# Performance work log

Hardware: AMD Instinct MI355X
Metric: run time of the kernel (lower is better)

The kernel has to match this reference:

```python
import jax, jax.numpy as jnp
import numpy as np

N = 50000          # num nodes
E = 600000         # num edges
D_IN = 128         # node_dim
D_HID = 128        # hidden_dim
D_OUT = 32         # num_classes
R = 32             # num_relations
B = 8              # num_bases


def setup_inputs() -> dict:
    key = jax.random.key(0)
    ks = jax.random.split(key, 12)
    inp = {
        "x": jax.random.normal(ks[0], (N, D_IN), dtype=jnp.float32),
        "V1": jax.random.normal(ks[1], (B, D_IN, D_HID), dtype=jnp.float32) * 0.05,
        "a1": jax.random.normal(ks[2], (R, B), dtype=jnp.float32),
        "root1": jax.random.normal(ks[3], (D_IN, D_HID), dtype=jnp.float32) * 0.05,
        "bias1": jnp.zeros((D_HID,), dtype=jnp.float32),
        "V2": jax.random.normal(ks[4], (B, D_HID, D_OUT), dtype=jnp.float32) * 0.05,
        "a2": jax.random.normal(ks[5], (R, B), dtype=jnp.float32),
        "root2": jax.random.normal(ks[6], (D_HID, D_OUT), dtype=jnp.float32) * 0.05,
        "bias2": jnp.zeros((D_OUT,), dtype=jnp.float32),
        "edge_index": jax.random.randint(ks[7], (2, E), 0, N, dtype=jnp.int64),
        "edge_type": jax.random.randint(ks[8], (E,), 0, R, dtype=jnp.int64),
    }
    return inp


def rgcn_layer(x, V, a, root, bias, src, dst, etype):
    # Aggregate neighbor features per (relation, dst-node) with mean norm,
    # then apply basis-decomposed relation weights W_r = sum_b a[r,b] V_b.
    D = x.shape[-1]
    seg = etype * N + dst                                   # [E] combined segment id
    msgs = x[src]                                           # [E, D] gather
    agg = jax.ops.segment_sum(msgs, seg, num_segments=R * N)        # [R*N, D]
    cnt = jax.ops.segment_sum(jnp.ones((msgs.shape[0], 1), x.dtype), seg,
                              num_segments=R * N)                   # [R*N, 1]
    agg = (agg / jnp.maximum(cnt, 1.0)).reshape(R, N, D)            # [R, N, D]
    W = jnp.einsum('rb,bdo->rdo', a, V)                     # [R, D, Dout]
    out = jnp.einsum('rnd,rdo->no', agg, W) + x @ root + bias
    return out


def reference(x, V1, a1, root1, bias1, V2, a2, root2, bias2, edge_index, edge_type):
    src, dst = edge_index[0], edge_index[1]
    h = rgcn_layer(x, V1, a1, root1, bias1, src, dst, edge_type)
    h = jax.nn.relu(h)
    h = rgcn_layer(h, V2, a2, root2, bias2, src, dst, edge_type)
    return jax.nn.softmax(h, axis=1)
```

## Files before the change

kernel.cpp:

```cpp
#include <hip/hip_runtime.h>
#include <hip/hip_bf16.h>


typedef __attribute__((ext_vector_type(8))) short bf16x8;
typedef __attribute__((ext_vector_type(4))) float f32x4;
typedef unsigned short u16;

constexpr int TD   = 128;
constexpr int TB   = 8;
constexpr int TK   = TB * TD;
constexpr int TNB  = 16;
constexpr int BLK  = 512;
constexpr int ZK   = TK + 8;
constexpr int XK   = TD + 8;

__device__ inline void splitbf(float v, u16& h, u16& l) {
  unsigned int u = __float_as_uint(v);
  unsigned int r = u + 0x7FFF + ((u >> 16) & 1);
  u16 hb = (u16)(r >> 16);
  float hv = __uint_as_float((unsigned int)hb << 16);
  float lo = v - hv;
  unsigned int u2 = __float_as_uint(lo);
  unsigned int r2 = u2 + 0x7FFF + ((u2 >> 16) & 1);
  h = hb;
  l = (u16)(r2 >> 16);
}

__global__ void k_prep(const float* __restrict__ V1, const float* __restrict__ root1,
                       const float* __restrict__ V2, const float* __restrict__ root2,
                       u16* __restrict__ v1th, u16* __restrict__ v1tl,
                       u16* __restrict__ r1th, u16* __restrict__ r1tl,
                       u16* __restrict__ v2th, u16* __restrict__ v2tl,
                       u16* __restrict__ r2th, u16* __restrict__ r2tl) {
  int idx = blockIdx.x * 256 + threadIdx.x;
  if (idx < 128 * 1024) splitbf(V1[(size_t)(idx & 1023) * 128 + (idx >> 10)], v1th[idx], v1tl[idx]);
  if (idx < 128 * 128)  splitbf(root1[(size_t)(idx & 127) * 128 + (idx >> 7)], r1th[idx], r1tl[idx]);
  if (idx < 32 * 1024)  splitbf(V2[(size_t)(idx & 1023) * 32 + (idx >> 10)], v2th[idx], v2tl[idx]);
  if (idx < 32 * 128)   splitbf(root2[(size_t)(idx & 127) * 32 + (idx >> 7)], r2th[idx], r2tl[idx]);
}

__global__ void k_hist(const int* __restrict__ ei, const int* __restrict__ et,
                       int* __restrict__ deg, int* __restrict__ cnt2,
                       int E, int N) {
  int e = blockIdx.x * 256 + threadIdx.x;
  if (e >= E) return;
  int d = ei[E + e];
  int r = et[e];
  atomicAdd(&deg[d], 1);
  atomicAdd(&cnt2[r * N + d], 1);
}

__global__ void k_scan(const int* __restrict__ deg, int* __restrict__ off,
                       int* __restrict__ cursor, int n, int total) {
  __shared__ int wsum[16];
  __shared__ int carry_s;
  const int t = threadIdx.x, lane = t & 63, w = t >> 6;
  if (t == 0) carry_s = 0;
  __syncthreads();
  for (int base = 0; base < n; base += 1024) {
    int i = base + t;
    int v = (i < n) ? deg[i] : 0;
    int s = v;
#pragma unroll
    for (int d = 1; d < 64; d <<= 1) {
      int u = __shfl_up(s, d);
      if (lane >= d) s += u;
    }
    if (lane == 63) wsum[w] = s;
    __syncthreads();
    if (w == 0) {
      int ws = (lane < 16) ? wsum[lane] : 0;
#pragma unroll
      for (int d = 1; d < 16; d <<= 1) {
        int u = __shfl_up(ws, d);
        if (lane >= d) ws += u;
      }
      if (lane < 16) wsum[lane] = ws;
    }
    __syncthreads();
    int wbase = (w == 0) ? 0 : wsum[w - 1];
    int carry = carry_s;
    if (i < n) { int ex = carry + wbase + s - v; off[i] = ex; cursor[i] = ex; }
    __syncthreads();
    if (t == 1023) carry_s = carry + wbase + s;
    __syncthreads();
  }
  if (t == 0) off[n] = total;
}

__global__ void k_scatter(const int* __restrict__ ei, const int* __restrict__ et,
                          int* __restrict__ cursor, const int* __restrict__ cnt2,
                          int* __restrict__ packed, float* __restrict__ invc,
                          int E, int N) {
  int e = blockIdx.x * 256 + threadIdx.x;
  if (e >= E) return;
  int s = ei[e], d = ei[E + e], r = et[e];
  int p = atomicAdd(&cursor[d], 1);
  packed[p] = s | (r << 17);
  invc[p] = 1.0f / (float)cnt2[r * N + d];
}

#define MFMA16(A, B, C) __builtin_amdgcn_mfma_f32_16x16x32_bf16((A), (B), (C), 0, 0, 0)

template <int DOUT, bool RELU, bool SOFTMAX>
__global__ __launch_bounds__(BLK, 4) void k_layer(
    const float* __restrict__ in,
    const u16* __restrict__ wth, const u16* __restrict__ wtl,
    const float* __restrict__ a,
    const u16* __restrict__ rth, const u16* __restrict__ rtl,
    const float* __restrict__ bias, const int* __restrict__ off,
    const int* __restrict__ packed, const float* __restrict__ invc,
    float* __restrict__ out, int Ntot) {
  extern __shared__ char smem[];
  u16* zh = (u16*)smem;
  u16* zl = zh + TNB * ZK;
  u16* xh = zl + TNB * ZK;
  u16* xl2 = xh + TNB * XK;
  float* ash = (float*)(xl2 + TNB * XK);
  const int t = threadIdx.x;
  const int n0 = blockIdx.x * TNB;

  if (t < 256) ash[t] = a[t];
  {
    int row = t >> 5;
    int c4 = (t & 31) * 4;
    int n = n0 + row;
    float4 v = make_float4(0.f, 0.f, 0.f, 0.f);
    if (n < Ntot) v = *reinterpret_cast<const float4*>(in + (size_t)n * TD + c4);
    u16 h0, l0;
    splitbf(v.x, h0, l0); xh[row * XK + c4]     = h0; xl2[row * XK + c4]     = l0;
    splitbf(v.y, h0, l0); xh[row * XK + c4 + 1] = h0; xl2[row * XK + c4 + 1] = l0;
    splitbf(v.z, h0, l0); xh[row * XK + c4 + 2] = h0; xl2[row * XK + c4 + 2] = l0;
    splitbf(v.w, h0, l0); xh[row * XK + c4 + 3] = h0; xl2[row * XK + c4 + 3] = l0;
  }
  __syncthreads();

  {
    const int wv = t >> 6, lane = t & 63;
    for (int nn = wv * 2; nn < wv * 2 + 2; ++nn) {
      int n = n0 + nn;
      float zacc[16];
#pragma unroll
      for (int j = 0; j < 16; ++j) zacc[j] = 0.f;
      if (n < Ntot) {
        int e = off[n], e1 = off[n + 1];
        for (; e + 2 <= e1; e += 2) {
          int pk0 = packed[e], pk1 = packed[e + 1];
          float iv0 = invc[e], iv1 = invc[e + 1];
          int s0 = pk0 & 131071, r0 = pk0 >> 17;
          int s1 = pk1 & 131071, r1 = pk1 >> 17;
          float x00 = in[(size_t)s0 * TD + lane];
          float x01 = in[(size_t)s0 * TD + 64 + lane];
          float x10 = in[(size_t)s1 * TD + lane];
          float x11 = in[(size_t)s1 * TD + 64 + lane];
          const float* ar0 = ash + r0 * TB;
          const float* ar1 = ash + r1 * TB;
#pragma unroll
          for (int b = 0; b < TB; ++b) {
            float c0 = ar0[b] * iv0;
            float c1 = ar1[b] * iv1;
            zacc[2 * b]     += c0 * x00;
            zacc[2 * b + 1] += c0 * x01;
            zacc[2 * b]     += c1 * x10;
            zacc[2 * b + 1] += c1 * x11;
          }
        }
        if (e < e1) {
          int pk = packed[e];
          float iv = invc[e];
          int s = pk & 131071, r = pk >> 17;
          float xv0 = in[(size_t)s * TD + lane];
          float xv1 = in[(size_t)s * TD + 64 + lane];
          const float* ar = ash + r * TB;
#pragma unroll
          for (int b = 0; b < TB; ++b) {
            float c = ar[b] * iv;
            zacc[2 * b]     += c * xv0;
            zacc[2 * b + 1] += c * xv1;
          }
        }
      }
#pragma unroll
      for (int b = 0; b < TB; ++b) {
        u16 h0, l0, h1, l1;
        splitbf(zacc[2 * b], h0, l0);
        splitbf(zacc[2 * b + 1], h1, l1);
        zh[nn * ZK + b * TD + lane]      = h0;
        zl[nn * ZK + b * TD + lane]      = l0;
        zh[nn * ZK + b * TD + 64 + lane] = h1;
        zl[nn * ZK + b * TD + 64 + lane] = l1;
      }
    }
  }
  __syncthreads();

  const int w = t >> 6, lane = t & 63;
  const int mc = lane & 15, kg = lane >> 4;

  if constexpr (DOUT == 128) {
    f32x4 acc = {0.f, 0.f, 0.f, 0.f};
    {
      const u16* za = zh + mc * ZK + kg * 8;
      const u16* zb = zl + mc * ZK + kg * 8;
      const u16* bha = wth + (size_t)(w * 16 + mc) * TK + kg * 8;
      const u16* bla = wtl + (size_t)(w * 16 + mc) * TK + kg * 8;
#pragma unroll 4
      for (int ks = 0; ks < 32; ++ks) {
        bf16x8 ah  = *(const bf16x8*)(za + 32 * ks);
        bf16x8 alo = *(const bf16x8*)(zb + 32 * ks);
        bf16x8 bh  = *(const bf16x8*)(bha + 32 * ks);
        bf16x8 blo = *(const bf16x8*)(bla + 32 * ks);
        acc = MFMA16(ah, bh, acc);
        acc = MFMA16(alo, bh, acc);
        acc = MFMA16(ah, blo, acc);
      }
      const u16* xa = xh + mc * XK + kg * 8;
      const u16* xb = xl2 + mc * XK + kg * 8;
      const u16* rha = rth + (size_t)(w * 16 + mc) * TD + kg * 8;
      const u16* rla = rtl + (size_t)(w * 16 + mc) * TD + kg * 8;
#pragma unroll
      for (int ks = 0; ks < 4; ++ks) {
        bf16x8 ah  = *(const bf16x8*)(xa + 32 * ks);
        bf16x8 alo = *(const bf16x8*)(xb + 32 * ks);
        bf16x8 bh  = *(const bf16x8*)(rha + 32 * ks);
        bf16x8 blo = *(const bf16x8*)(rla + 32 * ks);
        acc = MFMA16(ah, bh, acc);
        acc = MFMA16(alo, bh, acc);
        acc = MFMA16(ah, blo, acc);
      }
    }
    float bb = bias[w * 16 + mc];
#pragma unroll
    for (int j = 0; j < 4; ++j) {
      int n = n0 + kg * 4 + j;
      if (n < Ntot) {
        float v = acc[j] + bb;
        if (RELU) v = fmaxf(v, 0.f);
        out[(size_t)n * 128 + w * 16 + mc] = v;
      }
    }
  } else {
    f32x4 a0 = {0.f, 0.f, 0.f, 0.f}, a1 = {0.f, 0.f, 0.f, 0.f};
    {
      const u16* za = zh + mc * ZK + kg * 8;
      const u16* zb = zl + mc * ZK + kg * 8;
      const u16* b0h = wth + (size_t)mc * TK + kg * 8;
      const u16* b0l = wtl + (size_t)mc * TK + kg * 8;
      const u16* b1h = wth + (size_t)(16 + mc) * TK + kg * 8;
      const u16* b1l = wtl + (size_t)(16 + mc) * TK + kg * 8;
#pragma unroll
      for (int i = 0; i < 4; ++i) {
        int ks = w * 4 + i;
        bf16x8 ah  = *(const bf16x8*)(za + 32 * ks);
        bf16x8 alo = *(const bf16x8*)(zb + 32 * ks);
        bf16x8 bh0 = *(const bf16x8*)(b0h + 32 * ks);
        bf16x8 bl0 = *(const bf16x8*)(b0l + 32 * ks);
        bf16x8 bh1 = *(const bf16x8*)(b1h + 32 * ks);
        bf16x8 bl1 = *(const bf16x8*)(b1l + 32 * ks);
        a0 = MFMA16(ah, bh0, a0);
        a0 = MFMA16(alo, bh0, a0);
        a0 = MFMA16(ah, bl0, a0);
        a1 = MFMA16(ah, bh1, a1);
        a1 = MFMA16(alo, bh1, a1);
        a1 = MFMA16(ah, bl1, a1);
      }
      if (w < 4) {
        int ks = w;
        bf16x8 ah  = *(const bf16x8*)(xh + mc * XK + kg * 8 + 32 * ks);
        bf16x8 alo = *(const bf16x8*)(xl2 + mc * XK + kg * 8 + 32 * ks);
        bf16x8 bh0 = *(const bf16x8*)(rth + (size_t)mc * TD + kg * 8 + 32 * ks);
        bf16x8 bl0 = *(const bf16x8*)(rtl + (size_t)mc * TD + kg * 8 + 32 * ks);
        bf16x8 bh1 = *(const bf16x8*)(rth + (size_t)(16 + mc) * TD + kg * 8 + 32 * ks);
        bf16x8 bl1 = *(const bf16x8*)(rtl + (size_t)(16 + mc) * TD + kg * 8 + 32 * ks);
        a0 = MFMA16(ah, bh0, a0);
        a0 = MFMA16(alo, bh0, a0);
        a0 = MFMA16(ah, bl0, a0);
        a1 = MFMA16(ah, bh1, a1);
        a1 = MFMA16(alo, bh1, a1);
        a1 = MFMA16(ah, bl1, a1);
      }
    }
    __syncthreads();
    float* pc = (float*)smem;
#pragma unroll
    for (int j = 0; j < 4; ++j) {
      pc[(w * 2 + 0) * 256 + (kg * 4 + j) * 16 + mc] = a0[j];
      pc[(w * 2 + 1) * 256 + (kg * 4 + j) * 16 + mc] = a1[j];
    }
    __syncthreads();
    int row = t >> 5, col = t & 31;
    int tile = col >> 4, cc = col & 15;
    float v = 0.f;
#pragma unroll
    for (int ww = 0; ww < 8; ++ww) v += pc[(ww * 2 + tile) * 256 + row * 16 + cc];
    v += bias[col];
    if constexpr (SOFTMAX) {
      float m = v;
      m = fmaxf(m, __shfl_xor(m, 1));
      m = fmaxf(m, __shfl_xor(m, 2));
      m = fmaxf(m, __shfl_xor(m, 4));
      m = fmaxf(m, __shfl_xor(m, 8));
      m = fmaxf(m, __shfl_xor(m, 16));
      float ev = __expf(v - m);
      float s = ev;
      s += __shfl_xor(s, 1); s += __shfl_xor(s, 2); s += __shfl_xor(s, 4);
      s += __shfl_xor(s, 8); s += __shfl_xor(s, 16);
      v = ev / s;
    }
    int n = n0 + row;
    if (n < Ntot) out[(size_t)n * 32 + col] = v;
  }
}

extern "C" void kernel_launch(void* const* d_in, const int* in_sizes, int n_in,
                              void* d_out, int out_size, void* d_ws, size_t ws_size,
                              hipStream_t stream) {
  const float* x     = (const float*)d_in[0];
  const float* V1    = (const float*)d_in[1];
  const float* a1    = (const float*)d_in[2];
  const float* root1 = (const float*)d_in[3];
  const float* bias1 = (const float*)d_in[4];
  const float* V2    = (const float*)d_in[5];
  const float* a2    = (const float*)d_in[6];
  const float* root2 = (const float*)d_in[7];
  const float* bias2 = (const float*)d_in[8];
  const int*   ei    = (const int*)d_in[9];
  const int*   et    = (const int*)d_in[10];

  const int N = in_sizes[0] / TD;
  const int E = in_sizes[10];
  const int R = 32;

  char* w = (char*)d_ws;
  auto alloc = [&](size_t bytes) {
    char* p = w;
    w += (bytes + 255) & ~(size_t)255;
    return p;
  };
  int*   off    = (int*)alloc((size_t)(N + 1) * 4);
  int*   cursor = (int*)alloc((size_t)N * 4);
  int*   deg    = (int*)alloc((size_t)N * 4);
  int*   cnt2   = (int*)alloc((size_t)R * N * 4);
  int*   packed = (int*)alloc((size_t)E * 4);
  float* invc   = (float*)alloc((size_t)E * 4);
  float* h      = (float*)alloc((size_t)N * TD * 4);
  u16*   v1th   = (u16*)alloc((size_t)128 * 1024 * 2);
  u16*   v1tl   = (u16*)alloc((size_t)128 * 1024 * 2);
  u16*   r1th   = (u16*)alloc((size_t)128 * 128 * 2);
  u16*   r1tl   = (u16*)alloc((size_t)128 * 128 * 2);
  u16*   v2th   = (u16*)alloc((size_t)32 * 1024 * 2);
  u16*   v2tl   = (u16*)alloc((size_t)32 * 1024 * 2);
  u16*   r2th   = (u16*)alloc((size_t)32 * 128 * 2);
  u16*   r2tl   = (u16*)alloc((size_t)32 * 128 * 2);

  hipMemsetAsync(deg, 0, (size_t)N * 4, stream);
  hipMemsetAsync(cnt2, 0, (size_t)R * N * 4, stream);

  k_prep<<<512, 256, 0, stream>>>(V1, root1, V2, root2,
                                  v1th, v1tl, r1th, r1tl, v2th, v2tl, r2th, r2tl);

  int egrid = (E + 255) / 256;
  k_hist<<<egrid, 256, 0, stream>>>(ei, et, deg, cnt2, E, N);
  k_scan<<<1, 1024, 0, stream>>>(deg, off, cursor, N, E);
  k_scatter<<<egrid, 256, 0, stream>>>(ei, et, cursor, cnt2, packed, invc, E, N);

  const size_t shmem = (size_t)(2 * TNB * ZK + 2 * TNB * XK) * 2 + 256 * 4;
  hipFuncSetAttribute(reinterpret_cast<const void*>(&k_layer<128, true, false>),
                      hipFuncAttributeMaxDynamicSharedMemorySize, (int)shmem);
  hipFuncSetAttribute(reinterpret_cast<const void*>(&k_layer<32, false, true>),
                      hipFuncAttributeMaxDynamicSharedMemorySize, (int)shmem);

  int ngrid = (N + TNB - 1) / TNB;
  k_layer<128, true, false><<<ngrid, BLK, shmem, stream>>>(
      x, v1th, v1tl, a1, r1th, r1tl, bias1, off, packed, invc, h, N);
  k_layer<32, false, true><<<ngrid, BLK, shmem, stream>>>(
      h, v2th, v2tl, a2, r2th, r2tl, bias2, off, packed, invc, (float*)d_out, N);
}
```

Measured before the change: 579.7 us.

## Split wavefront across two edges with float4 gathers and software-pipelined loads

The per-node aggregation now has each half-wavefront handle a different edge, each lane loading a float4 of the source row instead of two scalars. Loads for the next pair of edges are issued before the current pair is computed, and the two halves are combined with a cross-lane shuffle before the bf16 hi/lo split. The Z tile is then written to shared memory as packed 4-element vectors. This targets gather latency and load-instruction count in the edge loop, at the cost of twice the accumulator registers and an extra reduction step.

```diff
diff --git a/kernel.cpp b/kernel.cpp
--- a/kernel.cpp
+++ b/kernel.cpp
@@ -5,6 +5,7 @@
 typedef __attribute__((ext_vector_type(8))) short bf16x8;
 typedef __attribute__((ext_vector_type(4))) float f32x4;
 typedef unsigned short u16;
+typedef __attribute__((ext_vector_type(4))) unsigned short u16x4;
 
 constexpr int TD   = 128;
 constexpr int TB   = 8;
@@ -14,16 +15,15 @@
 constexpr int ZK   = TK + 8;
 constexpr int XK   = TD + 8;
 
-__device__ inline void splitbf(float v, u16& h, u16& l) {
+__device__ inline unsigned int splitbf(float v) {
   unsigned int u = __float_as_uint(v);
   unsigned int r = u + 0x7FFF + ((u >> 16) & 1);
-  u16 hb = (u16)(r >> 16);
-  float hv = __uint_as_float((unsigned int)hb << 16);
+  unsigned int hb = r >> 16;
+  float hv = __uint_as_float(hb << 16);
   float lo = v - hv;
   unsigned int u2 = __float_as_uint(lo);
   unsigned int r2 = u2 + 0x7FFF + ((u2 >> 16) & 1);
-  h = hb;
-  l = (u16)(r2 >> 16);
+  return (hb & 0xFFFFu) | (r2 & 0xFFFF0000u);
 }
 
 __global__ void k_prep(const float* __restrict__ V1, const float* __restrict__ root1,
@@ -33,10 +33,22 @@
                        u16* __restrict__ v2th, u16* __restrict__ v2tl,
                        u16* __restrict__ r2th, u16* __restrict__ r2tl) {
   int idx = blockIdx.x * 256 + threadIdx.x;
-  if (idx < 128 * 1024) splitbf(V1[(size_t)(idx & 1023) * 128 + (idx >> 10)], v1th[idx], v1tl[idx]);
-  if (idx < 128 * 128)  splitbf(root1[(size_t)(idx & 127) * 128 + (idx >> 7)], r1th[idx], r1tl[idx]);
-  if (idx < 32 * 1024)  splitbf(V2[(size_t)(idx & 1023) * 32 + (idx >> 10)], v2th[idx], v2tl[idx]);
-  if (idx < 32 * 128)   splitbf(root2[(size_t)(idx & 127) * 32 + (idx >> 7)], r2th[idx], r2tl[idx]);
+  if (idx < 128 * 1024) {
+    unsigned int p = splitbf(V1[(size_t)(idx & 1023) * 128 + (idx >> 10)]);
+    v1th[idx] = (u16)p; v1tl[idx] = (u16)(p >> 16);
+  }
+  if (idx < 128 * 128) {
+    unsigned int p = splitbf(root1[(size_t)(idx & 127) * 128 + (idx >> 7)]);
+    r1th[idx] = (u16)p; r1tl[idx] = (u16)(p >> 16);
+  }
+  if (idx < 32 * 1024) {
+    unsigned int p = splitbf(V2[(size_t)(idx & 1023) * 32 + (idx >> 10)]);
+    v2th[idx] = (u16)p; v2tl[idx] = (u16)(p >> 16);
+  }
+  if (idx < 32 * 128) {
+    unsigned int p = splitbf(root2[(size_t)(idx & 127) * 32 + (idx >> 7)]);
+    r2th[idx] = (u16)p; r2tl[idx] = (u16)(p >> 16);
+  }
 }
 
 __global__ void k_hist(const int* __restrict__ ei, const int* __restrict__ et,
@@ -127,68 +139,87 @@
     int n = n0 + row;
     float4 v = make_float4(0.f, 0.f, 0.f, 0.f);
     if (n < Ntot) v = *reinterpret_cast<const float4*>(in + (size_t)n * TD + c4);
-    u16 h0, l0;
-    splitbf(v.x, h0, l0); xh[row * XK + c4]     = h0; xl2[row * XK + c4]     = l0;
-    splitbf(v.y, h0, l0); xh[row * XK + c4 + 1] = h0; xl2[row * XK + c4 + 1] = l0;
-    splitbf(v.z, h0, l0); xh[row * XK + c4 + 2] = h0; xl2[row * XK + c4 + 2] = l0;
-    splitbf(v.w, h0, l0); xh[row * XK + c4 + 3] = h0; xl2[row * XK + c4 + 3] = l0;
+    unsigned int p0 = splitbf(v.x), p1 = splitbf(v.y), p2 = splitbf(v.z), p3 = splitbf(v.w);
+    xh[row * XK + c4]     = (u16)p0; xl2[row * XK + c4]     = (u16)(p0 >> 16);
+    xh[row * XK + c4 + 1] = (u16)p1; xl2[row * XK + c4 + 1] = (u16)(p1 >> 16);
+    xh[row * XK + c4 + 2] = (u16)p2; xl2[row * XK + c4 + 2] = (u16)(p2 >> 16);
+    xh[row * XK + c4 + 3] = (u16)p3; xl2[row * XK + c4 + 3] = (u16)(p3 >> 16);
   }
   __syncthreads();
 
   {
     const int wv = t >> 6, lane = t & 63;
+    const int hf = lane >> 5, q = lane & 31;
+
     for (int nn = wv * 2; nn < wv * 2 + 2; ++nn) {
       int n = n0 + nn;
-      float zacc[16];
-#pragma unroll
-      for (int j = 0; j < 16; ++j) zacc[j] = 0.f;
+      float acc[8][4];
+#pragma unroll
+      for (int b = 0; b < 8; ++b)
+#pragma unroll
+        for (int j = 0; j < 4; ++j) acc[b][j] = 0.f;
+
       if (n < Ntot) {
-        int e = off[n], e1 = off[n + 1];
-        for (; e + 2 <= e1; e += 2) {
-          int pk0 = packed[e], pk1 = packed[e + 1];
-          float iv0 = invc[e], iv1 = invc[e + 1];
-          int s0 = pk0 & 131071, r0 = pk0 >> 17;
-          int s1 = pk1 & 131071, r1 = pk1 >> 17;
-          float x00 = in[(size_t)s0 * TD + lane];
-          float x01 = in[(size_t)s0 * TD + 64 + lane];
-          float x10 = in[(size_t)s1 * TD + lane];
-          float x11 = in[(size_t)s1 * TD + 64 + lane];
-          const float* ar0 = ash + r0 * TB;
-          const float* ar1 = ash + r1 * TB;
-#pragma unroll
-          for (int b = 0; b < TB; ++b) {
-            float c0 = ar0[b] * iv0;
-            float c1 = ar1[b] * iv1;
-            zacc[2 * b]     += c0 * x00;
-            zacc[2 * b + 1] += c0 * x01;
-            zacc[2 * b]     += c1 * x10;
-            zacc[2 * b + 1] += c1 * x11;
+        int e0 = off[n], e1 = off[n + 1];
+        int np = (e1 - e0 + 1) >> 1;
+
+        struct Pk { float4 xv, c0, c1; };
+        auto ldst = [&](int pe) {
+          Pk P;
+          int e = e0 + 2 * pe + hf;
+          float iv = 0.f; int r = 0;
+          P.xv = make_float4(0.f, 0.f, 0.f, 0.f);
+          if (e < e1) {
+            int pk = packed[e];
+            iv = invc[e];
+            r = pk >> 17;
+            P.xv = *reinterpret_cast<const float4*>(in + (size_t)(pk & 131071) * TD + q * 4);
+          }
+          float4 t0 = *reinterpret_cast<const float4*>(ash + r * 8);
+          float4 t1 = *reinterpret_cast<const float4*>(ash + r * 8 + 4);
+          P.c0 = make_float4(t0.x * iv, t0.y * iv, t0.z * iv, t0.w * iv);
+          P.c1 = make_float4(t1.x * iv, t1.y * iv, t1.z * iv, t1.w * iv);
+          return P;
+        };
+        auto comp = [&](const Pk& P) {
+#define ACCB(bi, cc) \
+          acc[bi][0] += (cc) * P.xv.x; acc[bi][1] += (cc) * P.xv.y; \
+          acc[bi][2] += (cc) * P.xv.z; acc[bi][3] += (cc) * P.xv.w;
+          ACCB(0, P.c0.x) ACCB(1, P.c0.y) ACCB(2, P.c0.z) ACCB(3, P.c0.w)
+          ACCB(4, P.c1.x) ACCB(5, P.c1.y) ACCB(6, P.c1.z) ACCB(7, P.c1.w)
+#undef ACCB
+        };
+
+        Pk A, B;
+        if (np > 0) A = ldst(0);
+        if (np > 1) B = ldst(1);
+        for (int pe = 0; pe < np; pe += 2) {
+          comp(A);
+          if (pe + 2 < np) A = ldst(pe + 2);
+          if (pe + 1 < np) {
+            comp(B);
+            if (pe + 3 < np) B = ldst(pe + 3);
           }
         }
-        if (e < e1) {
-          int pk = packed[e];
-          float iv = invc[e];
-          int s = pk & 131071, r = pk >> 17;
-          float xv0 = in[(size_t)s * TD + lane];
-          float xv1 = in[(size_t)s * TD + 64 + lane];
-          const float* ar = ash + r * TB;
-#pragma unroll
-          for (int b = 0; b < TB; ++b) {
-            float c = ar[b] * iv;
-            zacc[2 * b]     += c * xv0;
-            zacc[2 * b + 1] += c * xv1;
-          }
+      }
+
+#pragma unroll
+      for (int b = 0; b < 8; ++b) {
+        float v0 = acc[b][0] + __shfl_xor(acc[b][0], 32);
+        float v1 = acc[b][1] + __shfl_xor(acc[b][1], 32);
+        float v2 = acc[b][2] + __shfl_xor(acc[b][2], 32);
+        float v3 = acc[b][3] + __shfl_xor(acc[b][3], 32);
+        if (hf == 0) {
+          unsigned int p0 = splitbf(v0), p1 = splitbf(v1), p2 = splitbf(v2), p3 = splitbf(v3);
+          u16x4 hh, ll;
+          hh[0] = (u16)p0; ll[0] = (u16)(p0 >> 16);
+          hh[1] = (u16)p1; ll[1] = (u16)(p1 >> 16);
+          hh[2] = (u16)p2; ll[2] = (u16)(p2 >> 16);
+          hh[3] = (u16)p3; ll[3] = (u16)(p3 >> 16);
+          int idx = nn * ZK + b * TD + q * 4;
+          *reinterpret_cast<u16x4*>(zh + idx) = hh;
+          *reinterpret_cast<u16x4*>(zl + idx) = ll;
         }
-      }
-#pragma unroll
-      for (int b = 0; b < TB; ++b) {
-        u16 h0, l0, h1, l1;
-        splitbf(zacc[2 * b], h0, l0);
-        splitbf(zacc[2 * b + 1], h1, l1);
-        zh[nn * ZK + b * TD + lane]      = h0;
-        zl[nn * ZK + b * TD + lane]      = l0;
-        zh[nn * ZK + b * TD + 64 + lane] = h1;
-        zl[nn * ZK + b * TD + 64 + lane] = l1;
       }
     }
   }
@@ -365,10 +396,10 @@
   k_scatter<<<egrid, 256, 0, stream>>>(ei, et, cursor, cnt2, packed, invc, E, N);
 
   const size_t shmem = (size_t)(2 * TNB * ZK + 2 * TNB * XK) * 2 + 256 * 4;
-  hipFuncSetAttribute(reinterpret_cast<const void*>(&k_layer<128, true, false>),
-                      hipFuncAttributeMaxDynamicSharedMemorySize, (int)shmem);
-  hipFuncSetAttribute(reinterpret_cast<const void*>(&k_layer<32, false, true>),
-                      hipFuncAttributeMaxDynamicSharedMemorySize, (int)shmem);
+  (void)hipFuncSetAttribute(reinterpret_cast<const void*>(&k_layer<128, true, false>),
+                            hipFuncAttributeMaxDynamicSharedMemorySize, (int)shmem);
+  (void)hipFuncSetAttribute(reinterpret_cast<const void*>(&k_layer<32, false, true>),
+                            hipFuncAttributeMaxDynamicSharedMemorySize, (int)shmem);
 
   int ngrid = (N + TNB - 1) / TNB;
   k_layer<128, true, false><<<ngrid, BLK, shmem, stream>>>(
```

Measured after the change: 564.6 us. -2.6%, faster.
